# Optimization experiments

Measured on AMD Instinct MI355X. Metric: run time of the kernel, lower is better.

Reference implementation:

```python
import jax, jax.numpy as jnp
import numpy as np

NEG_INF = -9e15
ALPHA = 0.2  # LeakyReLU negative slope

N, IN_F, OUT_F = 8192, 512, 64


def setup_inputs() -> dict:
    key = jax.random.key(0)
    k1, k2, k3, k4 = jax.random.split(key, 4)
    input = jax.random.normal(k1, (N, IN_F), dtype=jnp.float32)
    adj = jax.random.randint(k2, (N, N), 0, 2, dtype=jnp.int32)
    init_range = float(np.sqrt(6.0 / (IN_F + OUT_F)))
    W = jax.random.uniform(k3, (IN_F, OUT_F), dtype=jnp.float32,
                           minval=-init_range, maxval=init_range)
    a_range = float(np.sqrt(6.0 / (2 * OUT_F + 1)))
    a = jax.random.uniform(k4, (2 * OUT_F, 1), dtype=jnp.float32,
                           minval=-a_range, maxval=a_range)
    return {"input": input, "adj": adj, "W": W, "a": a}


def reference(input, adj, W, a):
    h = input @ W                      # [N, F']
    a_left, a_right = a[:OUT_F], a[OUT_F:]   # each [F', 1]
    att_l = h @ a_left                 # [N, 1]
    att_r = h @ a_right                # [N, 1]
    e = jax.nn.leaky_relu(att_l + att_r.T, negative_slope=ALPHA)  # [N, N]
    e = jnp.where(adj == 0, jnp.float32(NEG_INF), e)
    attention = jax.nn.softmax(e, axis=1)
    # dropout is identity in eval mode (training=False)
    h_prime = attention @ h            # [N, F']
    return jax.nn.elu(h_prime)         # concat=True -> ELU activation
```

## Files before the change

### kernel.cpp

```cpp
#include <hip/hip_runtime.h>
#include <stdint.h>

#define ALPHA 0.2f
#define LOG2E 1.44269504088896340736f

typedef __attribute__((ext_vector_type(8))) short bf16x8;
typedef __attribute__((ext_vector_type(4))) float f32x4;

__device__ __forceinline__ unsigned short f2bf(float f) {
    unsigned u = __builtin_bit_cast(unsigned, f);
    u += 0x7fffu + ((u >> 16) & 1u);
    return (unsigned short)(u >> 16);
}
__device__ __forceinline__ float bf2f(unsigned short h) {
    unsigned u = ((unsigned)h) << 16;
    return __builtin_bit_cast(float, u);
}
__device__ __forceinline__ unsigned f2ord(float f) {
    unsigned b = __builtin_bit_cast(unsigned, f);
    return (b & 0x80000000u) ? ~b : (b | 0x80000000u);
}
__device__ __forceinline__ float ord2f(unsigned k) {
    unsigned b = (k & 0x80000000u) ? (k & 0x7fffffffu) : ~k;
    return __builtin_bit_cast(float, b);
}

__global__ __launch_bounds__(256) void gat_h(
    const float* __restrict__ input, const float* __restrict__ W,
    float* __restrict__ h)
{
    __shared__ float x_lds[16 * 128];
    const int tid = threadIdx.x;
    const int i0  = (blockIdx.x >> 2) * 16;
    const int k0  = (blockIdx.x & 3) * 128;

    {
        const int r  = tid >> 4;
        const int jc = (tid & 15) * 8;
        const float* src = input + (size_t)(i0 + r) * 512 + k0 + jc;
        *(f32x4*)&x_lds[r * 128 + jc]     = *(const f32x4*)src;
        *(f32x4*)&x_lds[r * 128 + jc + 4] = *(const f32x4*)(src + 4);
    }
    __syncthreads();

    const int c = tid & 63;
    const int w = tid >> 6;
    float acc[4] = {0.f, 0.f, 0.f, 0.f};
    const float* Wc = W + (size_t)k0 * 64 + c;
    #pragma unroll 4
    for (int kk = 0; kk < 128; kk += 4) {
        const float w0 = Wc[(kk+0)*64], w1 = Wc[(kk+1)*64];
        const float w2 = Wc[(kk+2)*64], w3 = Wc[(kk+3)*64];
        #pragma unroll
        for (int ri = 0; ri < 4; ++ri) {
            const f32x4 x = *(const f32x4*)&x_lds[(w + 4*ri) * 128 + kk];
            acc[ri] += x.x * w0 + x.y * w1 + x.z * w2 + x.w * w3;
        }
    }
    #pragma unroll
    for (int ri = 0; ri < 4; ++ri)
        unsafeAtomicAdd(&h[(size_t)(i0 + w + 4*ri) * 64 + c], acc[ri]);
}

__global__ __launch_bounds__(256) void gat_aux(
    const float* __restrict__ h, const float* __restrict__ a,
    float* __restrict__ attL, float* __restrict__ attR,
    unsigned short* __restrict__ hPack, unsigned* __restrict__ wsR)
{
    __shared__ float hl[32 * 64];
    __shared__ unsigned rmax;
    const int tid = threadIdx.x;
    const int j0  = blockIdx.x * 32;
    if (tid == 0) rmax = 0u;

    {
        const float* src = h + (size_t)j0 * 64 + tid * 8;
        *(f32x4*)&hl[tid * 8]     = *(const f32x4*)src;
        *(f32x4*)&hl[tid * 8 + 4] = *(const f32x4*)(src + 4);
    }
    __syncthreads();

    {
        const int row = tid >> 3;
        const int cs  = (tid & 7) * 8;
        float pL = 0.f, pR = 0.f;
        #pragma unroll
        for (int u = 0; u < 8; ++u) {
            const float hv = hl[row * 64 + cs + u];
            pL += hv * a[cs + u];
            pR += hv * a[64 + cs + u];
        }
        pL += __shfl_xor(pL, 1, 64); pR += __shfl_xor(pR, 1, 64);
        pL += __shfl_xor(pL, 2, 64); pR += __shfl_xor(pR, 2, 64);
        pL += __shfl_xor(pL, 4, 64); pR += __shfl_xor(pR, 4, 64);
        if ((tid & 7) == 0) {
            attL[j0 + row] = pL;
            attR[j0 + row] = pR;
            atomicMax(&rmax, f2ord(pR));
        }
    }

    {
        const int g = tid >> 6;
        const int l = tid & 63;
        const int m = l & 15;
        const int q = l >> 4;
        bf16x8 v;
        #pragma unroll
        for (int u = 0; u < 8; ++u)
            v[u] = (short)f2bf(hl[(q * 8 + u) * 64 + g * 16 + m]);
        *(bf16x8*)&hPack[(size_t)(blockIdx.x * 4 + g) * 512 + l * 8] = v;
    }

    __syncthreads();
    if (tid == 0) atomicMax(wsR, rmax);
}

__global__ __launch_bounds__(256, 4) void gat_attn(
    const int* __restrict__ adj,
    const float* __restrict__ attL, const float* __restrict__ attR,
    const unsigned short* __restrict__ hPack, const unsigned* __restrict__ wsR,
    float* __restrict__ outAcc, float* __restrict__ lAcc)
{
    __shared__ unsigned smem[4096];
    __shared__ float l_lds[64];
    const int tid  = threadIdx.x;
    const int lane = tid & 63;
    const int wq   = tid >> 6;
    const int m    = lane & 15;
    const int quad = lane >> 4;
    const int ti   = blockIdx.x >> 2;
    const int q4   = blockIdx.x & 3;
    const int i0   = ti * 16;
    const int jc0  = q4 * 64 + wq * 16;

    {
        const int r    = tid >> 4;
        const int lidx = (tid & 3) * 16 + r;
        const int t    = (tid & 15) >> 2;
        unsigned char* bb = (unsigned char*)smem;
        const int* src = adj + (size_t)(i0 + r) * 8192 + q4 * 2048 + (tid & 15) * 8;
        #pragma unroll 4
        for (int it = 0; it < 16; ++it) {
            const int4 v0 = *(const int4*)(src + it * 128);
            const int4 v1 = *(const int4*)(src + it * 128 + 4);
            unsigned b = 0;
            b |= (v0.x != 0) << 0; b |= (v0.y != 0) << 1;
            b |= (v0.z != 0) << 2; b |= (v0.w != 0) << 3;
            b |= (v1.x != 0) << 4; b |= (v1.y != 0) << 5;
            b |= (v1.z != 0) << 6; b |= (v1.w != 0) << 7;
            bb[((((it >> 2) * 1024) + (it & 3) * 64 + lidx) << 2) + t] = (unsigned char)b;
        }
    }
    __syncthreads();

    unsigned abw[4];
    #pragma unroll
    for (int g4 = 0; g4 < 4; ++g4)
        abw[g4] = smem[wq * 1024 + g4 * 64 + lane];

    const float R   = ord2f(*wsR);
    const float a_l = attL[i0 + m];
    const float t0  = a_l + R;
    const float M   = fmaxf(t0, ALPHA * t0);
    const float mc  = M * LOG2E;

    const float*          ar_p = attR + jc0 * 32 + quad * 8;
    const unsigned short* hp_p = hPack + (size_t)jc0 * 4 * 512 + lane * 8;

    f32x4 acc[4];
    #pragma unroll
    for (int g = 0; g < 4; ++g) acc[g] = (f32x4){0.f, 0.f, 0.f, 0.f};
    float lsum = 0.f;

    #pragma unroll
    for (int jg = 0; jg < 4; ++jg) {
        const unsigned ab = abw[jg];
        #pragma unroll
        for (int t = 0; t < 4; ++t) {
            const int s = jg * 4 + t;
            const f32x4 r0 = *(const f32x4*)(ar_p + s * 32);
            const f32x4 r1 = *(const f32x4*)(ar_p + s * 32 + 4);
            bf16x8 B[4];
            #pragma unroll
            for (int g = 0; g < 4; ++g)
                B[g] = *(const bf16x8*)(hp_p + (size_t)(s * 4 + g) * 512);

            const unsigned bits = (ab >> (t * 8)) & 0xffu;
            const float tv[8] = { a_l + r0.x, a_l + r0.y, a_l + r0.z, a_l + r0.w,
                                  a_l + r1.x, a_l + r1.y, a_l + r1.z, a_l + r1.w };
            bf16x8 af;
            #pragma unroll
            for (int u = 0; u < 8; ++u) {
                const float e  = fmaxf(tv[u], ALPHA * tv[u]);
                const float pe = __builtin_amdgcn_exp2f(__builtin_fmaf(e, LOG2E, -mc));
                const float pv = (bits & (1u << u)) ? pe : 0.0f;
                const unsigned short pb = f2bf(pv);
                af[u] = (short)pb;
                lsum += bf2f(pb);
            }
            #pragma unroll
            for (int g = 0; g < 4; ++g)
                acc[g] = __builtin_amdgcn_mfma_f32_16x16x32_bf16(af, B[g], acc[g], 0, 0, 0);
        }
    }

    lsum += __shfl_xor(lsum, 16, 64);
    lsum += __shfl_xor(lsum, 32, 64);
    if (lane < 16) l_lds[wq * 16 + lane] = lsum;
    float* accf = (float*)smem;
    #pragma unroll
    for (int g = 0; g < 4; ++g)
        *(f32x4*)&accf[(wq * 64 + lane) * 16 + g * 4] = acc[g];
    __syncthreads();

    #pragma unroll
    for (int q = 0; q < 4; ++q) {
        const int e      = tid + q * 256;
        const int lane_e = e >> 4;
        const int k16    = e & 15;
        float s = 0.f;
        #pragma unroll
        for (int ww = 0; ww < 4; ++ww) s += accf[(ww * 64 + lane_e) * 16 + k16];
        const int row = (lane_e >> 4) * 4 + (k16 & 3);
        const int col = (k16 >> 2) * 16 + (lane_e & 15);
        unsafeAtomicAdd(&outAcc[(size_t)(i0 + row) * 64 + col], s);
    }
    if (tid < 16) {
        const float s = l_lds[tid] + l_lds[16 + tid] + l_lds[32 + tid] + l_lds[48 + tid];
        unsafeAtomicAdd(&lAcc[i0 + tid], s);
    }
}

__global__ __launch_bounds__(256) void gat_final(
    float* __restrict__ out, const float* __restrict__ lAcc)
{
    const int idx = blockIdx.x * 256 + threadIdx.x;
    const float v = out[idx] / lAcc[idx >> 6];
    out[idx] = v > 0.f ? v : (__builtin_amdgcn_exp2f(v * LOG2E) - 1.0f);
}

extern "C" void kernel_launch(void* const* d_in, const int* in_sizes, int n_in,
                              void* d_out, int out_size, void* d_ws, size_t ws_size,
                              hipStream_t stream) {
    const float* input = (const float*)d_in[0];
    const int*   adj   = (const int*)d_in[1];
    const float* W     = (const float*)d_in[2];
    const float* a     = (const float*)d_in[3];
    float* out = (float*)d_out;

    char* ws = (char*)d_ws;
    unsigned*       wsR   = (unsigned*)(ws + 0);
    float*          lAcc  = (float*)(ws + 4096);
    float*          h     = (float*)(ws + 36864);
    float*          attL  = (float*)(ws + 2134016);
    float*          attR  = (float*)(ws + 2166784);
    unsigned short* hPack = (unsigned short*)(ws + 2199552);

    hipMemsetAsync(d_out, 0, (size_t)out_size * sizeof(float), stream);
    hipMemsetAsync(d_ws, 0, 2134016, stream);

    gat_h    <<<2048, 256, 0, stream>>>(input, W, h);
    gat_aux  <<< 256, 256, 0, stream>>>(h, a, attL, attR, hPack, wsR);
    gat_attn <<<2048, 256, 0, stream>>>(adj, attL, attR, hPack, wsR, out, lAcc);
    gat_final<<<2048, 256, 0, stream>>>(out, lAcc);
}
```

Measured before the change: 417.0 us.

## Fuse h projection and attention-logit prep into one kernel

Merges the input@W projection and the auxiliary kernel (attention logits, max of attR, bf16 packing of h) into one kernel. Each block now computes all 512 k for 16 rows, so the split-K atomics into a global h buffer go away, and the memset of that buffer shrinks to the small header region. This removes one launch, the h round trip through global memory, and the atomic traffic. In exchange each block runs a longer serial K loop with a larger LDS footprint, and the grid drops to 512 blocks, which lowers parallelism for the matmul.

New measurement: 419.3 us. About the same (+0.5%).

```diff
diff --git a/kernel.cpp b/kernel.cpp
--- a/kernel.cpp
+++ b/kernel.cpp
@@ -25,68 +25,57 @@
     return __builtin_bit_cast(float, b);
 }
 
-__global__ __launch_bounds__(256) void gat_h(
+__global__ __launch_bounds__(256) void gat_pre(
     const float* __restrict__ input, const float* __restrict__ W,
-    float* __restrict__ h)
-{
-    __shared__ float x_lds[16 * 128];
-    const int tid = threadIdx.x;
-    const int i0  = (blockIdx.x >> 2) * 16;
-    const int k0  = (blockIdx.x & 3) * 128;
-
-    {
-        const int r  = tid >> 4;
-        const int jc = (tid & 15) * 8;
-        const float* src = input + (size_t)(i0 + r) * 512 + k0 + jc;
-        *(f32x4*)&x_lds[r * 128 + jc]     = *(const f32x4*)src;
-        *(f32x4*)&x_lds[r * 128 + jc + 4] = *(const f32x4*)(src + 4);
-    }
-    __syncthreads();
-
-    const int c = tid & 63;
-    const int w = tid >> 6;
-    float acc[4] = {0.f, 0.f, 0.f, 0.f};
-    const float* Wc = W + (size_t)k0 * 64 + c;
-    #pragma unroll 4
-    for (int kk = 0; kk < 128; kk += 4) {
-        const float w0 = Wc[(kk+0)*64], w1 = Wc[(kk+1)*64];
-        const float w2 = Wc[(kk+2)*64], w3 = Wc[(kk+3)*64];
-        #pragma unroll
-        for (int ri = 0; ri < 4; ++ri) {
-            const f32x4 x = *(const f32x4*)&x_lds[(w + 4*ri) * 128 + kk];
-            acc[ri] += x.x * w0 + x.y * w1 + x.z * w2 + x.w * w3;
-        }
-    }
-    #pragma unroll
-    for (int ri = 0; ri < 4; ++ri)
-        unsafeAtomicAdd(&h[(size_t)(i0 + w + 4*ri) * 64 + c], acc[ri]);
-}
-
-__global__ __launch_bounds__(256) void gat_aux(
-    const float* __restrict__ h, const float* __restrict__ a,
+    const float* __restrict__ a,
     float* __restrict__ attL, float* __restrict__ attR,
     unsigned short* __restrict__ hPack, unsigned* __restrict__ wsR)
 {
-    __shared__ float hl[32 * 64];
+    __shared__ float x_lds[16 * 512];
+    __shared__ float h_lds[16 * 64];
     __shared__ unsigned rmax;
     const int tid = threadIdx.x;
-    const int j0  = blockIdx.x * 32;
+    const int i0  = blockIdx.x * 16;
     if (tid == 0) rmax = 0u;
 
     {
-        const float* src = h + (size_t)j0 * 64 + tid * 8;
-        *(f32x4*)&hl[tid * 8]     = *(const f32x4*)src;
-        *(f32x4*)&hl[tid * 8 + 4] = *(const f32x4*)(src + 4);
+        const float* src = input + (size_t)i0 * 512;
+        #pragma unroll
+        for (int u = 0; u < 8; ++u) {
+            const int f = (u * 256 + tid) * 4;
+            *(f32x4*)&x_lds[f] = *(const f32x4*)(src + f);
+        }
     }
     __syncthreads();
 
     {
+        const int c = tid & 63;
+        const int w = tid >> 6;
+        float acc[4] = {0.f, 0.f, 0.f, 0.f};
+        const float* Wc = W + c;
+        #pragma unroll 4
+        for (int kk = 0; kk < 512; kk += 4) {
+            const float w0 = Wc[(kk+0)*64], w1 = Wc[(kk+1)*64];
+            const float w2 = Wc[(kk+2)*64], w3 = Wc[(kk+3)*64];
+            #pragma unroll
+            for (int ri = 0; ri < 4; ++ri) {
+                const f32x4 x = *(const f32x4*)&x_lds[(w + 4*ri) * 512 + kk];
+                acc[ri] += x.x * w0 + x.y * w1 + x.z * w2 + x.w * w3;
+            }
+        }
+        #pragma unroll
+        for (int ri = 0; ri < 4; ++ri)
+            h_lds[(w + 4*ri) * 64 + c] = acc[ri];
+    }
+    __syncthreads();
+
+    if (tid < 128) {
         const int row = tid >> 3;
         const int cs  = (tid & 7) * 8;
         float pL = 0.f, pR = 0.f;
         #pragma unroll
         for (int u = 0; u < 8; ++u) {
-            const float hv = hl[row * 64 + cs + u];
+            const float hv = h_lds[row * 64 + cs + u];
             pL += hv * a[cs + u];
             pR += hv * a[64 + cs + u];
         }
@@ -94,22 +83,22 @@
         pL += __shfl_xor(pL, 2, 64); pR += __shfl_xor(pR, 2, 64);
         pL += __shfl_xor(pL, 4, 64); pR += __shfl_xor(pR, 4, 64);
         if ((tid & 7) == 0) {
-            attL[j0 + row] = pL;
-            attR[j0 + row] = pR;
+            attL[i0 + row] = pL;
+            attR[i0 + row] = pR;
             atomicMax(&rmax, f2ord(pR));
         }
-    }
-
-    {
-        const int g = tid >> 6;
-        const int l = tid & 63;
-        const int m = l & 15;
-        const int q = l >> 4;
+    } else {
+        const int t2   = tid - 128;
+        const int g    = t2 >> 5;
+        const int qq   = (t2 >> 4) & 1;
+        const int m    = t2 & 15;
+        const int jb   = blockIdx.x >> 1;
+        const int half = blockIdx.x & 1;
         bf16x8 v;
         #pragma unroll
         for (int u = 0; u < 8; ++u)
-            v[u] = (short)f2bf(hl[(q * 8 + u) * 64 + g * 16 + m]);
-        *(bf16x8*)&hPack[(size_t)(blockIdx.x * 4 + g) * 512 + l * 8] = v;
+            v[u] = (short)f2bf(h_lds[(qq * 8 + u) * 64 + g * 16 + m]);
+        *(bf16x8*)&hPack[(size_t)(jb * 4 + g) * 512 + ((half * 2 + qq) * 16 + m) * 8] = v;
     }
 
     __syncthreads();
@@ -252,16 +241,14 @@
     char* ws = (char*)d_ws;
     unsigned*       wsR   = (unsigned*)(ws + 0);
     float*          lAcc  = (float*)(ws + 4096);
-    float*          h     = (float*)(ws + 36864);
     float*          attL  = (float*)(ws + 2134016);
     float*          attR  = (float*)(ws + 2166784);
     unsigned short* hPack = (unsigned short*)(ws + 2199552);
 
     hipMemsetAsync(d_out, 0, (size_t)out_size * sizeof(float), stream);
-    hipMemsetAsync(d_ws, 0, 2134016, stream);
-
-    gat_h    <<<2048, 256, 0, stream>>>(input, W, h);
-    gat_aux  <<< 256, 256, 0, stream>>>(h, a, attL, attR, hPack, wsR);
+    hipMemsetAsync(d_ws, 0, 36864, stream);
+
+    gat_pre  <<< 512, 256, 0, stream>>>(input, W, a, attL, attR, hPack, wsR);
     gat_attn <<<2048, 256, 0, stream>>>(adj, attL, attR, hPack, wsR, out, lAcc);
     gat_final<<<2048, 256, 0, stream>>>(out, lAcc);
 }
```
